# Kernel tuning notes

Measured on AMD Instinct MI355X. Metric: run time of the kernel, lower is better.

Reference implementation:

```python
import jax, jax.numpy as jnp
import numpy as np
import math

B, N, D, H, K, W = 2, 2048, 512, 8, 64, 5
HD = D // H      # head_dim = 64
QC = HD // 4     # per-head quaternion component = 16
QI = D // 4      # full-model quaternion component = 128


def _qlinear(x, r, i, j, k, b):
    # Hamilton-product weight matrix, as built in QLinear.forward
    Wm = jnp.concatenate([
        jnp.concatenate([r, -i, -j, -k], 1),
        jnp.concatenate([i,  r, -k,  j], 1),
        jnp.concatenate([j,  k,  r, -i], 1),
        jnp.concatenate([k, -j,  i,  r], 1)], 0)
    return x @ Wm.T + b


def _layernorm(x, g, b, eps=1e-5):
    m = x.mean(-1, keepdims=True)
    v = ((x - m) ** 2).mean(-1, keepdims=True)
    return (x - m) / jnp.sqrt(v + eps) * g + b


def _forward(query, key, value, cross_context, density_feat, mask, time_idx,
             q_r, q_i, q_j, q_k, q_b, k_r, k_i, k_j, k_k, k_b,
             v_w, v_b, o_w, o_b, thr, dm1_w, dm1_b, dm2_w, dm2_b,
             ef, ec, ev_w, ev_b, ln_g, ln_b):
    spike_slope = 5.0
    # ---- QuaternionSpikeAttention (cross_ctx=True, dropout inactive in eval) ----
    q = _qlinear(query, q_r, q_i, q_j, q_k, q_b)
    k = _qlinear(key, k_r, k_i, k_j, k_k, k_b) + _qlinear(cross_context, k_r, k_i, k_j, k_k, k_b)
    v = jnp.concatenate([value, cross_context], -1) @ v_w.T + v_b
    qh = q.reshape(B, N, H, HD)
    kh = k.reshape(B, N, H, HD)
    vh = v.reshape(B, N, H, HD)
    # sum of the 4 quaternion-component dot products == full dot over head_dim
    scores = jnp.einsum('bmhd,bnhd->bhmn', qh, kh) / math.sqrt(QC)
    scores = jnp.clip(scores, -6.0, 6.0)
    base_thr = jax.nn.softplus(thr)
    hdm = jax.nn.gelu(density_feat @ dm1_w.T + dm1_b, approximate=False)
    d_shift = (hdm @ dm2_w.T + dm2_b)[..., 0]                # [B, N]
    threshold = base_thr + d_shift[:, None, None, :] * 0.1   # varies over key index
    gate = jax.nn.sigmoid(spike_slope * (scores - threshold))
    mod = scores * (1.0 + 2.0 * gate)
    m2 = mask[:, None, :, None] * mask[:, None, None, :]     # [B,1,M,N] outer mask
    mod = jnp.where(m2 == 0, -10000.0, mod)
    wts = jax.nn.softmax(jnp.clip(mod, -30.0, 30.0), axis=-1)
    attn = jnp.einsum('bhmn,bnhd->bmhd', wts, vh).reshape(B, N, D)
    attn = attn @ o_w.T + o_b
    # ---- TemporalEventConvolution ----
    order = jnp.argsort(time_idx, axis=1)
    qs = jnp.take_along_axis(query, order[..., None], axis=1)
    ms = jnp.take_along_axis(mask, order, axis=1)
    half = W // 2
    qp = jnp.pad(qs, ((0, 0), (half, half), (0, 0)))
    qwin = jnp.stack([qp[:, w:w + N] for w in range(W)], axis=2)  # [B,N,W,D]
    # quaternion-split filter matching collapses to a full dot over D
    act = jnp.einsum('bnwd,kwd->bnk', qwin, ef) / math.sqrt(QI)
    act = jnp.where(ms[..., None] == 0, -10000.0, act)
    act = jax.nn.softmax(act, axis=-1)
    ctx = act @ ec                                            # [B,N,D]
    ctx = _layernorm(ctx @ ev_w.T + ev_b, ln_g, ln_b) * ms[..., None]
    inv = jnp.argsort(order, axis=1)
    ctx = jnp.take_along_axis(ctx, inv[..., None], axis=1) * mask[..., None]
    return attn + ctx


def setup_inputs() -> dict:
    key0 = jax.random.key(0)
    ks = jax.random.split(key0, 24)
    lim = math.sqrt(6.0 / (QI + QI))
    def xav(k):
        return jax.random.uniform(k, (QI, QI), jnp.float32, -lim, lim)
    def lin(k, o, i):
        l = math.sqrt(1.0 / i)
        return jax.random.uniform(k, (o, i), jnp.float32, -l, l)
    return {
        'query': jax.random.normal(ks[0], (B, N, D), jnp.float32),
        'key': jax.random.normal(ks[1], (B, N, D), jnp.float32),
        'value': jax.random.normal(ks[2], (B, N, D), jnp.float32),
        'cross_context': jax.random.normal(ks[3], (B, N, D), jnp.float32),
        'density_feat': jax.random.normal(ks[4], (B, N, 3), jnp.float32),
        'mask': jnp.ones((B, N), jnp.float32),
        'time_idx': jax.random.randint(ks[5], (B, N), 0, 1000000),
        'q_r': xav(ks[6]), 'q_i': xav(ks[7]), 'q_j': xav(ks[8]), 'q_k': xav(ks[9]),
        'q_b': jnp.zeros((D,), jnp.float32),
        'k_r': xav(ks[10]), 'k_i': xav(ks[11]), 'k_j': xav(ks[12]), 'k_k': xav(ks[13]),
        'k_b': jnp.zeros((D,), jnp.float32),
        'v_w': lin(ks[14], D, 2 * D), 'v_b': jnp.zeros((D,), jnp.float32),
        'o_w': lin(ks[15], D, D), 'o_b': jnp.zeros((D,), jnp.float32),
        'thr': jnp.float32(-1.0),
        'dm1_w': lin(ks[16], 16, 3), 'dm1_b': jnp.zeros((16,), jnp.float32),
        'dm2_w': jnp.zeros((1, 16), jnp.float32), 'dm2_b': jnp.zeros((1,), jnp.float32),
        'ef': jax.random.normal(ks[17], (K, W, D), jnp.float32) * 0.02,
        'ec': jax.random.normal(ks[18], (K, D), jnp.float32) * 0.02,
        'ev_w': lin(ks[19], D, D), 'ev_b': jnp.zeros((D,), jnp.float32),
        'ln_g': jnp.ones((D,), jnp.float32), 'ln_b': jnp.zeros((D,), jnp.float32),
    }


def reference(query, key, value, cross_context, density_feat, mask, time_idx,
              q_r, q_i, q_j, q_k, q_b, k_r, k_i, k_j, k_k, k_b,
              v_w, v_b, o_w, o_b, thr, dm1_w, dm1_b, dm2_w, dm2_b,
              ef, ec, ev_w, ev_b, ln_g, ln_b):
    return _forward(query, key, value, cross_context, density_feat, mask, time_idx,
                    q_r, q_i, q_j, q_k, q_b, k_r, k_i, k_j, k_k, k_b,
                    v_w, v_b, o_w, o_b, thr, dm1_w, dm1_b, dm2_w, dm2_b,
                    ef, ec, ev_w, ev_b, ln_g, ln_b)
```

## Files before the change

kernel.cpp:

```cpp
#include <hip/hip_runtime.h>
#include <math.h>

#define BB 2
#define NN 2048
#define DDIM 512
#define HH 8
#define HDIM 64
#define BN 4096

#define WS_WMQ   0
#define WS_WMK   262144
#define WS_THRK  524288
#define WS_ORDER 528384
#define WS_DKW   532480
#define WS_W5    1843200
#define WS_Q     2105344
#define WS_K     4202496
#define WS_V     6299648
#define PLANE_US 2097152

typedef short bf16x8 __attribute__((ext_vector_type(8)));
typedef float f32x4  __attribute__((ext_vector_type(4)));

__device__ __forceinline__ float4 ld4(const float* p) { return *(const float4*)p; }

__device__ __forceinline__ float red16_sum(float v) {
  v += __shfl_xor(v, 1, 64);
  v += __shfl_xor(v, 2, 64);
  v += __shfl_xor(v, 4, 64);
  v += __shfl_xor(v, 8, 64);
  return v;
}

__device__ __forceinline__ unsigned short f2bu(float f) {
  unsigned u = __float_as_uint(f);
  unsigned r = 0x7FFFu + ((u >> 16) & 1u);
  return (unsigned short)((u + r) >> 16);
}
__device__ __forceinline__ float bu2f(unsigned short u) {
  return __uint_as_float(((unsigned)u) << 16);
}
__device__ __forceinline__ void split2(float x, unsigned short& hi, unsigned short& lo) {
  hi = f2bu(x);
  lo = f2bu(x - bu2f(hi));
}

__global__ __launch_bounds__(256) void build_wm_kernel(
    const float* __restrict__ qr, const float* __restrict__ qi,
    const float* __restrict__ qj, const float* __restrict__ qk,
    const float* __restrict__ kr, const float* __restrict__ ki,
    const float* __restrict__ kj, const float* __restrict__ kk,
    unsigned short* __restrict__ wmqH, unsigned short* __restrict__ wmqL,
    unsigned short* __restrict__ wmkH, unsigned short* __restrict__ wmkL)
{
  int idx = blockIdx.x * 256 + threadIdx.x;
  int sel = idx >> 18;
  int r   = idx & 262143;
  int p = r >> 9, q = r & 511;
  int pb = p >> 7, qb = q >> 7, pr = p & 127, qc = q & 127;
  const int   comp_t[4][4] = {{0,1,2,3},{1,0,3,2},{2,3,0,1},{3,2,1,0}};
  const float sign_t[4][4] = {{1.f,-1.f,-1.f,-1.f},{1.f,1.f,-1.f,1.f},
                              {1.f,1.f,1.f,-1.f},{1.f,-1.f,1.f,1.f}};
  const float* cq[4] = {qr,qi,qj,qk};
  const float* ck[4] = {kr,ki,kj,kk};
  int c = comp_t[pb][qb];
  float s = sign_t[pb][qb];
  const float* src = sel ? ck[c] : cq[c];
  float v = s * src[pr*128 + qc];
  unsigned short hi, lo;
  split2(v, hi, lo);
  if (sel) { wmkH[r] = hi; wmkL[r] = lo; }
  else     { wmqH[r] = hi; wmqL[r] = lo; }
}

__global__ __launch_bounds__(256) void presplit_kernel(
    const float* __restrict__ src, int n4,
    unsigned short* __restrict__ hp, unsigned short* __restrict__ lp)
{
  int i = blockIdx.x * 256 + threadIdx.x;
  if (i >= n4) return;
  float4 v = ((const float4*)src)[i];
  ushort4 h, l;
  split2(v.x, h.x, l.x);  split2(v.y, h.y, l.y);
  split2(v.z, h.z, l.z);  split2(v.w, h.w, l.w);
  ((ushort4*)hp)[i] = h;
  ((ushort4*)lp)[i] = l;
}

__global__ __launch_bounds__(256) void rank_kernel(const int* __restrict__ tidx,
                                                   int* __restrict__ order)
{
  __shared__ int ts[NN];
  int b = blockIdx.y;
  for (int i = threadIdx.x; i < NN; i += 256) ts[i] = tidx[b*NN + i];
  __syncthreads();
  int i = blockIdx.x * 256 + threadIdx.x;
  int ti = ts[i];
  int rank = 0;
  #pragma unroll 4
  for (int j = 0; j < NN; j++) {
    int tj = ts[j];
    rank += (tj < ti || (tj == ti && j < i)) ? 1 : 0;
  }
  order[b*NN + rank] = i;
}

__global__ __launch_bounds__(256) void thr_kernel(
    const float* __restrict__ df, const float* __restrict__ dm1w,
    const float* __restrict__ dm1b, const float* __restrict__ dm2w,
    const float* __restrict__ dm2b, const float* __restrict__ thrp,
    int dm1b_bstride, float* __restrict__ thrK)
{
  int i = blockIdx.x * 256 + threadIdx.x;
  if (i >= BN) return;
  int b = i >> 11;
  const float* bb = dm1b + b*dm1b_bstride;
  float x0 = df[i*3+0], x1 = df[i*3+1], x2 = df[i*3+2];
  float acc = dm2b[0];
  #pragma unroll
  for (int j = 0; j < 16; j++) {
    float h = dm1w[j*3+0]*x0 + dm1w[j*3+1]*x1 + dm1w[j*3+2]*x2 + bb[j];
    h = 0.5f * h * (1.f + erff(h * 0.70710678118654752f));
    acc += h * dm2w[j];
  }
  float tv = thrp[0];
  float base = fmaxf(tv, 0.f) + log1pf(expf(-fabsf(tv)));
  thrK[i] = base + 0.1f * acc;
}

#define GSTR 72
template<int MODE, int OUT, int AP, int BP>
__global__ __launch_bounds__(256) void mgemm_kernel(
    const float* __restrict__ A0, const float* __restrict__ A1,
    const unsigned short* __restrict__ APh, const unsigned short* __restrict__ APl,
    const float* __restrict__ W,
    const unsigned short* __restrict__ BPh, const unsigned short* __restrict__ BPl,
    const float* __restrict__ bias,
    float bias_scale, float scale, float* __restrict__ out,
    int Ka, int N, int ldout)
{
  __shared__ __align__(16) unsigned short AHi[64*GSTR], ALo[64*GSTR];
  __shared__ __align__(16) unsigned short BHi[64*GSTR], BLo[64*GSTR];
  const int t = threadIdx.x;
  const int w = t >> 6, lane = t & 63;
  const int quad = lane >> 4, lm = lane & 15;
  const int m0 = blockIdx.x * 64, n0 = blockIdx.y * 64;
  const int lrr = t >> 4, ld = (t & 15) * 4;

  f32x4 acc[4];
  #pragma unroll
  for (int s = 0; s < 4; s++) acc[s] = (f32x4){0.f,0.f,0.f,0.f};

  for (int k0 = 0; k0 < Ka; k0 += 64) {
    __syncthreads();
    if (AP) {
      #pragma unroll
      for (int i = 0; i < 2; i++) {
        int c = t*2 + i;
        int row = c >> 3, c8 = (c & 7) * 8;
        int off = (m0 + row)*Ka + k0 + c8;
        *(uint4*)&AHi[row*GSTR + c8] = *(const uint4*)&APh[off];
        *(uint4*)&ALo[row*GSTR + c8] = *(const uint4*)&APl[off];
      }
    } else {
      #pragma unroll
      for (int p = 0; p < 4; p++) {
        int row = lrr + p*16;
        float4 av;
        if (MODE == 0) {
          av = ld4(&A0[(size_t)(m0+row)*Ka + k0 + ld]);
        } else if (MODE == 1) {
          float4 x = ld4(&A0[(m0+row)*512 + k0 + ld]);
          float4 y = ld4(&A1[(m0+row)*512 + k0 + ld]);
          av = make_float4(x.x+y.x, x.y+y.y, x.z+y.z, x.w+y.w);
        } else {
          int kg = k0 + ld;
          av = (kg < 512) ? ld4(&A0[(m0+row)*512 + kg])
                          : ld4(&A1[(m0+row)*512 + kg - 512]);
        }
        ushort4 hi, lo;
        split2(av.x, hi.x, lo.x);  split2(av.y, hi.y, lo.y);
        split2(av.z, hi.z, lo.z);  split2(av.w, hi.w, lo.w);
        *(ushort4*)&AHi[row*GSTR + ld] = hi;
        *(ushort4*)&ALo[row*GSTR + ld] = lo;
      }
    }
    if (BP) {
      #pragma unroll
      for (int i = 0; i < 2; i++) {
        int c = t*2 + i;
        int row = c >> 3, c8 = (c & 7) * 8;
        int brow = n0 + row;  if (brow > N-1) brow = N-1;
        int off = brow*Ka + k0 + c8;
        *(uint4*)&BHi[row*GSTR + c8] = *(const uint4*)&BPh[off];
        *(uint4*)&BLo[row*GSTR + c8] = *(const uint4*)&BPl[off];
      }
    } else {
      #pragma unroll
      for (int p = 0; p < 4; p++) {
        int row = lrr + p*16;
        int brow = n0 + row;  if (brow > N-1) brow = N-1;
        float4 wv = ld4(&W[(size_t)brow*Ka + k0 + ld]);
        ushort4 hi, lo;
        split2(wv.x, hi.x, lo.x);  split2(wv.y, hi.y, lo.y);
        split2(wv.z, hi.z, lo.z);  split2(wv.w, hi.w, lo.w);
        *(ushort4*)&BHi[row*GSTR + ld] = hi;
        *(ushort4*)&BLo[row*GSTR + ld] = lo;
      }
    }
    __syncthreads();
    #pragma unroll
    for (int ks = 0; ks < 2; ks++) {
      int arow = (w*16 + lm)*GSTR + ks*32 + quad*8;
      bf16x8 ah = *(const bf16x8*)&AHi[arow];
      bf16x8 al = *(const bf16x8*)&ALo[arow];
      #pragma unroll
      for (int sub = 0; sub < 4; sub++) {
        int baddr = (sub*16 + lm)*GSTR + ks*32 + quad*8;
        bf16x8 bh = *(const bf16x8*)&BHi[baddr];
        bf16x8 bl = *(const bf16x8*)&BLo[baddr];
        acc[sub] = __builtin_amdgcn_mfma_f32_16x16x32_bf16(ah, bh, acc[sub], 0, 0, 0);
        acc[sub] = __builtin_amdgcn_mfma_f32_16x16x32_bf16(ah, bl, acc[sub], 0, 0, 0);
        acc[sub] = __builtin_amdgcn_mfma_f32_16x16x32_bf16(al, bh, acc[sub], 0, 0, 0);
      }
    }
  }
  #pragma unroll
  for (int sub = 0; sub < 4; sub++) {
    int col = n0 + sub*16 + lm;
    if (col >= N) continue;
    float bv = bias ? bias[col] * bias_scale : 0.f;
    if (OUT == 0) {
      #pragma unroll
      for (int r = 0; r < 4; r++) {
        int row = m0 + w*16 + quad*4 + r;
        out[(size_t)row*ldout + col] = acc[sub][r]*scale + bv;
      }
    } else if (OUT == 1) {
      unsigned short* hp = (unsigned short*)out;
      unsigned short* lp = hp + (size_t)4096*ldout;
      #pragma unroll
      for (int r = 0; r < 4; r++) {
        int row = m0 + w*16 + quad*4 + r;
        unsigned short hv, lv;
        split2(acc[sub][r]*scale + bv, hv, lv);
        hp[(size_t)row*ldout + col] = hv;
        lp[(size_t)row*ldout + col] = lv;
      }
    } else {
      unsigned short* hp = (unsigned short*)out;
      unsigned short* lp = hp + (size_t)PLANE_US;
      int hcol = col >> 6, d = col & 63;
      int row0 = m0 + w*16 + quad*4;
      int bb2 = row0 >> 11, n = row0 & 2047;
      unsigned short h0,h1,h2,h3,l0,l1,l2,l3;
      split2(acc[sub][0]*scale + bv, h0, l0);
      split2(acc[sub][1]*scale + bv, h1, l1);
      split2(acc[sub][2]*scale + bv, h2, l2);
      split2(acc[sub][3]*scale + bv, h3, l3);
      size_t vidx = (((size_t)bb2*8 + hcol)*64 + d)*2048 + n;
      *(ushort4*)&hp[vidx] = make_ushort4(h0,h1,h2,h3);
      *(ushort4*)&lp[vidx] = make_ushort4(l0,l1,l2,l3);
    }
  }
}

__global__ __launch_bounds__(256) void t1a_kernel(const float* __restrict__ dkw,
    const int* __restrict__ order, int K, int W, float* __restrict__ w5raw)
{
  int idx = blockIdx.x * 256 + threadIdx.x;
  if (idx >= BN*K) return;
  int k  = idx % K;
  int bn = idx / K;
  int b = bn >> 11, r = bn & 2047;
  const int* ob = order + b*NN;
  int KW = K*W, half = W >> 1;
  float acc = 0.f;
  for (int w = 0; w < W; w++) {
    int rr = r + w - half;
    if (rr < 0 || rr >= NN) continue;
    acc += dkw[(size_t)(b*NN + ob[rr])*KW + k*W + w];
  }
  w5raw[(size_t)(b*NN + ob[r])*K + k] = acc;
}

__global__ __launch_bounds__(256) void t1b_kernel(const float* __restrict__ mask,
    int K, float* __restrict__ w5)
{
  int i = blockIdx.x * 256 + threadIdx.x;
  if (i >= BN) return;
  float* row = w5 + (size_t)i*K;
  if (mask[i] == 0.f) {
    float u = 1.f / (float)K;
    for (int k = 0; k < K; k++) row[k] = u;
    return;
  }
  float mx = -1e30f;
  for (int k = 0; k < K; k++) mx = fmaxf(mx, row[k]);
  float ss = 0.f;
  for (int k = 0; k < K; k++) { float e = __expf(row[k]-mx); row[k] = e; ss += e; }
  float inv = 1.f/ss;
  for (int k = 0; k < K; k++) row[k] *= inv;
}

__global__ __launch_bounds__(256) void ecv_kernel(const float* __restrict__ ec,
    const float* __restrict__ evw, int K, float* __restrict__ ecv)
{
  int idx = blockIdx.x * 256 + threadIdx.x;
  if (idx >= K*512) return;
  int k = idx >> 9, j = idx & 511;
  const float4* e4 = (const float4*)(ec + k*512);
  const float4* w4 = (const float4*)(evw + j*512);
  float acc = 0.f;
  for (int d = 0; d < 128; d++) {
    float4 a = e4[d], b = w4[d];
    acc += a.x*b.x + a.y*b.y + a.z*b.z + a.w*b.w;
  }
  ecv[k*512 + j] = acc;
}

__global__ __launch_bounds__(256) void t2p_kernel(const float* __restrict__ w5,
    const float* __restrict__ ecv, const float* __restrict__ evb,
    int K, float* __restrict__ ctx2)
{
  int idx = blockIdx.x * 256 + threadIdx.x;
  int bn = idx >> 7;
  int q4 = idx & 127;
  const float* wp = w5 + (size_t)bn*K;
  const float4* e4 = (const float4*)ecv;
  float4 bv = ((const float4*)evb)[q4];
  float4 acc = bv;
  for (int k = 0; k < K; k++) {
    float w = wp[k];
    float4 e = e4[k*128 + q4];
    acc.x += w*e.x; acc.y += w*e.y; acc.z += w*e.z; acc.w += w*e.w;
  }
  ((float4*)ctx2)[idx] = acc;
}

#define QSTR 72
__global__ __launch_bounds__(256) void attn_kernel(
    const unsigned short* __restrict__ QHi, const unsigned short* __restrict__ QLo,
    const unsigned short* __restrict__ KHp, const unsigned short* __restrict__ KLp,
    const unsigned short* __restrict__ VtHi, const unsigned short* __restrict__ VtLo,
    const float* __restrict__ thrK, const float* __restrict__ mask,
    unsigned short* __restrict__ AoutH, unsigned short* __restrict__ AoutL)
{
  __shared__ __align__(16) unsigned short KHs[64*QSTR];
  __shared__ __align__(16) unsigned short KLs[64*QSTR];
  __shared__ __align__(16) unsigned short VHs[64*QSTR];
  __shared__ __align__(16) unsigned short VLs[64*QSTR];
  __shared__ float thr_s[64], mk_s[64], mm_s[32];
  __shared__ float ls[2][32];

  const int t = threadIdx.x;
  const int wv = t >> 6, lane = t & 63;
  const int g = wv & 1, sh = wv >> 1;
  const int quad = lane >> 4, lm = lane & 15;
  const int m0 = blockIdx.x * 32;
  const int bh = blockIdx.y;
  const int b = bh >> 3, h = bh & 7;
  const int base = b*NN*DDIM + h*HDIM;
  const int sr = t >> 3;
  const int sc = (t & 7) * 8;

  bf16x8 qh[2], ql[2];
  {
    size_t qoff = (size_t)(b*NN + m0 + g*16 + lm)*DDIM + h*HDIM + quad*8;
    qh[0] = *(const bf16x8*)&QHi[qoff];
    qh[1] = *(const bf16x8*)&QHi[qoff + 32];
    ql[0] = *(const bf16x8*)&QLo[qoff];
    ql[1] = *(const bf16x8*)&QLo[qoff + 32];
  }
  if (t < 32) mm_s[t] = mask[b*NN + m0 + t];

  f32x4 o_acc[2];
  o_acc[0] = (f32x4){0.f,0.f,0.f,0.f};
  o_acc[1] = (f32x4){0.f,0.f,0.f,0.f};
  float lsum[4] = {0.f,0.f,0.f,0.f};

  for (int n0 = 0; n0 < NN; n0 += 64) {
    __syncthreads();
    #pragma unroll
    for (int p = 0; p < 2; p++) {
      int row = sr + p*32;
      size_t gg = (size_t)(b*NN + n0 + row)*DDIM + h*HDIM + sc;
      *(uint4*)&KHs[row*QSTR + sc] = *(const uint4*)&KHp[gg];
      *(uint4*)&KLs[row*QSTR + sc] = *(const uint4*)&KLp[gg];
      size_t gv = ((size_t)bh*HDIM + row)*NN + n0 + sc;
      *(uint4*)&VHs[row*QSTR + sc] = *(const uint4*)&VtHi[gv];
      *(uint4*)&VLs[row*QSTR + sc] = *(const uint4*)&VtLo[gv];
    }
    if (t < 64) { thr_s[t] = thrK[b*NN + n0 + t]; mk_s[t] = mask[b*NN + n0 + t]; }
    __syncthreads();

    f32x4 s_acc[2];
    s_acc[0] = (f32x4){0.f,0.f,0.f,0.f};
    s_acc[1] = (f32x4){0.f,0.f,0.f,0.f};
    #pragma unroll
    for (int ks = 0; ks < 2; ks++) {
      #pragma unroll
      for (int sl = 0; sl < 2; sl++) {
        int sub = sh*2 + sl;
        int baddr = (sub*16 + lm)*QSTR + ks*32 + quad*8;
        bf16x8 bh8 = *(const bf16x8*)&KHs[baddr];
        bf16x8 bl8 = *(const bf16x8*)&KLs[baddr];
        s_acc[sl] = __builtin_amdgcn_mfma_f32_16x16x32_bf16(qh[ks], bh8, s_acc[sl], 0, 0, 0);
        s_acc[sl] = __builtin_amdgcn_mfma_f32_16x16x32_bf16(qh[ks], bl8, s_acc[sl], 0, 0, 0);
        s_acc[sl] = __builtin_amdgcn_mfma_f32_16x16x32_bf16(ql[ks], bh8, s_acc[sl], 0, 0, 0);
      }
    }
    __syncthreads();

    float thc5[2], mkc[2];
    #pragma unroll
    for (int sl = 0; sl < 2; sl++) {
      int key = (sh*2 + sl)*16 + lm;
      thc5[sl] = 5.f * thr_s[key];
      mkc[sl] = mk_s[key];
    }
    float p_[4][2];
    #pragma unroll
    for (int r = 0; r < 4; r++) {
      float mm = mm_s[g*16 + quad*4 + r];
      #pragma unroll
      for (int sl = 0; sl < 2; sl++) {
        float sc2 = s_acc[sl][r]*0.25f;
        sc2 = fminf(fmaxf(sc2,-6.f),6.f);
        float e = __expf(__builtin_fmaf(-5.f, sc2, thc5[sl]));
        float gte = __builtin_amdgcn_rcpf(1.f + e);
        float mv = sc2*(1.f + 2.f*gte);
        if (mm*mkc[sl] == 0.f) mv = -1e4f;
        mv = fminf(fmaxf(mv,-30.f),30.f);
        float p = __expf(mv - 30.f);
        p_[r][sl] = p;
        lsum[r] += p;
      }
    }
    #pragma unroll
    for (int r = 0; r < 4; r++) {
      int prow = (g*16 + quad*4 + r)*QSTR;
      int xk = quad << 3;
      #pragma unroll
      for (int sl = 0; sl < 2; sl++) {
        int cx = (lm + (sh*2+sl)*16) ^ xk;
        unsigned short hi, lo;
        split2(p_[r][sl], hi, lo);
        KHs[prow + cx] = hi;
        KLs[prow + cx] = lo;
      }
    }
    __syncthreads();

    bf16x8 ph[2], pl[2];
    {
      int arow = (g*16 + lm)*QSTR;
      int rk = ((lm >> 2) & 3) << 3;
      int c0 = (quad*8) ^ rk;
      int c1 = (quad*8 + 32) ^ rk;
      ph[0] = *(const bf16x8*)&KHs[arow + c0];
      ph[1] = *(const bf16x8*)&KHs[arow + c1];
      pl[0] = *(const bf16x8*)&KLs[arow + c0];
      pl[1] = *(const bf16x8*)&KLs[arow + c1];
    }
    #pragma unroll
    for (int ks = 0; ks < 2; ks++) {
      #pragma unroll
      for (int sl = 0; sl < 2; sl++) {
        int sub = sh*2 + sl;
        int baddr = (sub*16 + lm)*QSTR + ks*32 + quad*8;
        bf16x8 vh8 = *(const bf16x8*)&VHs[baddr];
        bf16x8 vl8 = *(const bf16x8*)&VLs[baddr];
        o_acc[sl] = __builtin_amdgcn_mfma_f32_16x16x32_bf16(ph[ks], vh8, o_acc[sl], 0, 0, 0);
        o_acc[sl] = __builtin_amdgcn_mfma_f32_16x16x32_bf16(ph[ks], vl8, o_acc[sl], 0, 0, 0);
        o_acc[sl] = __builtin_amdgcn_mfma_f32_16x16x32_bf16(pl[ks], vh8, o_acc[sl], 0, 0, 0);
      }
    }
  }

  __syncthreads();
  #pragma unroll
  for (int r = 0; r < 4; r++) {
    float s = red16_sum(lsum[r]);
    if (lm == 0) ls[sh][g*16 + quad*4 + r] = s;
  }
  __syncthreads();
  float inv[4];
  #pragma unroll
  for (int r = 0; r < 4; r++) {
    int rl = g*16 + quad*4 + r;
    inv[r] = 1.f / (ls[0][rl] + ls[1][rl]);
  }
  #pragma unroll
  for (int sl = 0; sl < 2; sl++) {
    #pragma unroll
    for (int r = 0; r < 4; r++) {
      int row = m0 + g*16 + quad*4 + r;
      float val = o_acc[sl][r] * inv[r];
      unsigned short hv, lv;
      split2(val, hv, lv);
      size_t o = (size_t)base + (size_t)row*DDIM + (sh*2+sl)*16 + lm;
      AoutH[o] = hv;
      AoutL[o] = lv;
    }
  }
}

__global__ __launch_bounds__(256) void t3_kernel(const float* __restrict__ ctx2,
    const float* __restrict__ lng, const float* __restrict__ lnb,
    const float* __restrict__ mask, const float* __restrict__ outf,
    float* __restrict__ out)
{
  int wid = threadIdx.x >> 6, lane = threadIdx.x & 63;
  int row = blockIdx.x * 4 + wid;
  const float4* x4 = (const float4*)(ctx2 + row*DDIM);
  float4 v0 = x4[lane], v1 = x4[lane+64];
  float s = v0.x+v0.y+v0.z+v0.w + v1.x+v1.y+v1.z+v1.w;
  #pragma unroll
  for (int m = 1; m < 64; m <<= 1) s += __shfl_xor(s, m, 64);
  float mean = s * (1.f/512.f);
  float d0 = v0.x-mean, d1 = v0.y-mean, d2 = v0.z-mean, d3 = v0.w-mean;
  float d4 = v1.x-mean, d5 = v1.y-mean, d6 = v1.z-mean, d7 = v1.w-mean;
  float sq = d0*d0+d1*d1+d2*d2+d3*d3+d4*d4+d5*d5+d6*d6+d7*d7;
  #pragma unroll
  for (int m = 1; m < 64; m <<= 1) sq += __shfl_xor(sq, m, 64);
  float rstd = rsqrtf(sq * (1.f/512.f) + 1e-5f);
  float mk = mask[row];
  float f = mk*mk;
  const float4* g4 = (const float4*)lng;
  const float4* b4 = (const float4*)lnb;
  float4 G0 = g4[lane], G1 = g4[lane+64], B0 = b4[lane], B1 = b4[lane+64];
  float4 O0 = *(const float4*)&outf[row*DDIM + lane*4];
  float4 O1 = *(const float4*)&outf[row*DDIM + (lane+64)*4];
  float4 R0, R1;
  R0.x = O0.x + (d0*rstd*G0.x + B0.x)*f;
  R0.y = O0.y + (d1*rstd*G0.y + B0.y)*f;
  R0.z = O0.z + (d2*rstd*G0.z + B0.z)*f;
  R0.w = O0.w + (d3*rstd*G0.w + B0.w)*f;
  R1.x = O1.x + (d4*rstd*G1.x + B1.x)*f;
  R1.y = O1.y + (d5*rstd*G1.y + B1.y)*f;
  R1.z = O1.z + (d6*rstd*G1.z + B1.z)*f;
  R1.w = O1.w + (d7*rstd*G1.w + B1.w)*f;
  *(float4*)&out[row*DDIM + lane*4] = R0;
  *(float4*)&out[row*DDIM + (lane+64)*4] = R1;
}

__global__ void telem_write_kernel(float val, float* __restrict__ out)
{
  if (threadIdx.x == 0 && blockIdx.x == 0) out[0] = val;
}

extern "C" void kernel_launch(void* const* d_in, const int* in_sizes, int n_in,
                              void* d_out, int out_size, void* d_ws, size_t ws_size,
                              hipStream_t stream)
{
  (void)n_in; (void)out_size; (void)ws_size;
  const float* query = (const float*)d_in[0];
  const float* key_  = (const float*)d_in[1];
  const float* value = (const float*)d_in[2];
  const float* cross = (const float*)d_in[3];
  const float* df    = (const float*)d_in[4];
  const float* mask  = (const float*)d_in[5];
  const int*   tidx  = (const int*)  d_in[6];
  const float* q_r = (const float*)d_in[7],  *q_i = (const float*)d_in[8];
  const float* q_j = (const float*)d_in[9],  *q_k = (const float*)d_in[10];
  const float* q_b = (const float*)d_in[11];
  const float* k_r = (const float*)d_in[12], *k_i = (const float*)d_in[13];
  const float* k_j = (const float*)d_in[14], *k_k = (const float*)d_in[15];
  const float* k_b = (const float*)d_in[16];
  const float* v_w = (const float*)d_in[17], *v_b = (const float*)d_in[18];
  const float* o_w = (const float*)d_in[19], *o_b = (const float*)d_in[20];
  const float* thrp = (const float*)d_in[21];
  const float* dm1w = (const float*)d_in[22], *dm1b = (const float*)d_in[23];
  const float* dm2w = (const float*)d_in[24], *dm2b = (const float*)d_in[25];
  const float* ef   = (const float*)d_in[26], *ec   = (const float*)d_in[27];
  const float* ev_w = (const float*)d_in[28], *ev_b = (const float*)d_in[29];
  const float* lng  = (const float*)d_in[30], *lnb  = (const float*)d_in[31];

  const int s23 = in_sizes[23];
  const int s26 = in_sizes[26];
  const int s27 = in_sizes[27];
  int Kf = (s27 > 0 && s27 % 512 == 0) ? s27 / 512 : 0;
  int Wf = (Kf > 0 && s26 % (Kf*512) == 0) ? s26 / (Kf*512) : 0;
  bool cfg_ok = (Kf >= 1 && Kf <= 64) && (Wf == 1 || Wf == 3 || Wf == 5)
                && (Kf*Wf <= 320);
  if (!cfg_ok) { Kf = 5; Wf = 5; }
  const int KW = Kf * Wf;
  const int dm1b_bstride = (s23 == 32) ? 16 : 0;

  float* ws   = (float*)d_ws;
  float* thrK = ws + WS_THRK;
  int*   order = (int*)(ws + WS_ORDER);
  float* dkw  = ws + WS_DKW;
  float* w5   = ws + WS_W5;
  float* Qb   = ws + WS_Q;
  float* Kb   = ws + WS_K;
  float* Vb   = ws + WS_V;
  float* out  = (float*)d_out;
  float* OutF = Kb;
  float* ctx2 = Qb;

  unsigned short* wmqH = (unsigned short*)(ws + WS_WMQ);
  unsigned short* wmqL = wmqH + 262144;
  unsigned short* wmkH = (unsigned short*)(ws + WS_WMK);
  unsigned short* wmkL = wmkH + 262144;
  unsigned short* qryH = (unsigned short*)d_out;
  unsigned short* qryL = qryH + PLANE_US;
  unsigned short* vwH  = (unsigned short*)(ws + WS_DKW);
  unsigned short* vwL  = vwH + 524288;
  unsigned short* owH  = (unsigned short*)(ws + WS_W5);
  unsigned short* owL  = owH + 262144;
  unsigned short* efH  = (unsigned short*)(ws + WS_WMQ);
  unsigned short* efL  = efH + KW*512;
  float* ecv = ws + WS_WMQ;

  const unsigned short* QHi = (const unsigned short*)Qb;
  const unsigned short* QLo = QHi + PLANE_US;
  const unsigned short* KHp = (const unsigned short*)Kb;
  const unsigned short* KLp = KHp + PLANE_US;
  const unsigned short* VtH = (const unsigned short*)Vb;
  const unsigned short* VtL = VtH + PLANE_US;

  build_wm_kernel<<<2048, 256, 0, stream>>>(q_r,q_i,q_j,q_k, k_r,k_i,k_j,k_k,
                                            wmqH, wmqL, wmkH, wmkL);
  rank_kernel<<<dim3(8,2), 256, 0, stream>>>(tidx, order);
  thr_kernel<<<16, 256, 0, stream>>>(df, dm1w, dm1b, dm2w, dm2b, thrp,
                                     dm1b_bstride, thrK);
  presplit_kernel<<<2048, 256, 0, stream>>>(query, 524288, qryH, qryL);
  presplit_kernel<<<512, 256, 0, stream>>>(v_w, 131072, vwH, vwL);
  presplit_kernel<<<256, 256, 0, stream>>>(o_w, 65536, owH, owL);

  const float rs128 = 0.08838834764831845f;
  mgemm_kernel<0,1,1,1><<<dim3(64,8), 256, 0, stream>>>(
      nullptr, nullptr, qryH, qryL, nullptr, wmqH, wmqL, q_b, 1.f, 1.f, Qb, 512, 512, 512);
  mgemm_kernel<1,1,0,1><<<dim3(64,8), 256, 0, stream>>>(
      key_, cross, nullptr, nullptr, nullptr, wmkH, wmkL, k_b, 2.f, 1.f, Kb, 512, 512, 512);
  presplit_kernel<<<(KW*128 + 255)/256, 256, 0, stream>>>(ef, KW*128, efH, efL);
  mgemm_kernel<2,2,0,1><<<dim3(64,8), 256, 0, stream>>>(
      value, cross, nullptr, nullptr, nullptr, vwH, vwL, v_b, 1.f, 1.f, Vb, 1024, 512, 512);
  mgemm_kernel<0,0,1,1><<<dim3(64,(KW+63)/64), 256, 0, stream>>>(
      nullptr, nullptr, qryH, qryL, nullptr, efH, efL, nullptr, 0.f, rs128, dkw, 512, KW, KW);

  attn_kernel<<<dim3(64,16), 256, 0, stream>>>(QHi, QLo, KHp, KLp, VtH, VtL,
                                               thrK, mask, qryH, qryL);
  mgemm_kernel<0,0,1,1><<<dim3(64,8), 256, 0, stream>>>(
      nullptr, nullptr, qryH, qryL, nullptr, owH, owL, o_b, 1.f, 1.f, OutF, 512, 512, 512);

  t1a_kernel<<<(BN*Kf + 255)/256, 256, 0, stream>>>(dkw, order, Kf, Wf, w5);
  t1b_kernel<<<16, 256, 0, stream>>>(mask, Kf, w5);
  ecv_kernel<<<(Kf*512 + 255)/256, 256, 0, stream>>>(ec, ev_w, Kf, ecv);
  t2p_kernel<<<2048, 256, 0, stream>>>(w5, ecv, ev_b, Kf, ctx2);
  t3_kernel<<<1024, 256, 0, stream>>>(ctx2, lng, lnb, mask, OutF, out);

  if (!cfg_ok) {
    int K2 = (s27 / 512 < 127) ? s27 / 512 : 127;
    telem_write_kernel<<<1, 64, 0, stream>>>(-65536.f * (float)(K2+1), out);
  }
}
```

Before: 546.1 us.

## Register-prefetch next tiles in GEMM and attention loops

Both the split-bf16 GEMM kernel and the attention kernel now load the next K-tile (and V/threshold/mask tiles) from global memory into registers while the current tile is being computed from LDS. The stores to shared memory happen at the top of each iteration from the prefetched registers. This hides global-load latency behind MFMA work, at the cost of more registers per thread and a possible drop in occupancy.

```diff
diff --git a/kernel.cpp b/kernel.cpp
--- a/kernel.cpp
+++ b/kernel.cpp
@@ -147,36 +147,75 @@
   const int m0 = blockIdx.x * 64, n0 = blockIdx.y * 64;
   const int lrr = t >> 4, ld = (t & 15) * 4;
 
-  f32x4 acc[4];
-  #pragma unroll
-  for (int s = 0; s < 4; s++) acc[s] = (f32x4){0.f,0.f,0.f,0.f};
-
-  for (int k0 = 0; k0 < Ka; k0 += 64) {
-    __syncthreads();
+  uint4  raH[2], raL[2];
+  float4 rfA[4], rfA2[4];
+  uint4  rbH[2], rbL[2];
+  float4 rfB[4];
+
+  auto loadA = [&](int kk) {
     if (AP) {
       #pragma unroll
       for (int i = 0; i < 2; i++) {
         int c = t*2 + i;
         int row = c >> 3, c8 = (c & 7) * 8;
-        int off = (m0 + row)*Ka + k0 + c8;
-        *(uint4*)&AHi[row*GSTR + c8] = *(const uint4*)&APh[off];
-        *(uint4*)&ALo[row*GSTR + c8] = *(const uint4*)&APl[off];
+        int off = (m0 + row)*Ka + kk + c8;
+        raH[i] = *(const uint4*)&APh[off];
+        raL[i] = *(const uint4*)&APl[off];
       }
     } else {
       #pragma unroll
       for (int p = 0; p < 4; p++) {
         int row = lrr + p*16;
-        float4 av;
         if (MODE == 0) {
-          av = ld4(&A0[(size_t)(m0+row)*Ka + k0 + ld]);
+          rfA[p] = ld4(&A0[(size_t)(m0+row)*Ka + kk + ld]);
         } else if (MODE == 1) {
-          float4 x = ld4(&A0[(m0+row)*512 + k0 + ld]);
-          float4 y = ld4(&A1[(m0+row)*512 + k0 + ld]);
-          av = make_float4(x.x+y.x, x.y+y.y, x.z+y.z, x.w+y.w);
+          rfA[p]  = ld4(&A0[(m0+row)*512 + kk + ld]);
+          rfA2[p] = ld4(&A1[(m0+row)*512 + kk + ld]);
         } else {
-          int kg = k0 + ld;
-          av = (kg < 512) ? ld4(&A0[(m0+row)*512 + kg])
-                          : ld4(&A1[(m0+row)*512 + kg - 512]);
+          int kg = kk + ld;
+          rfA[p] = (kg < 512) ? ld4(&A0[(m0+row)*512 + kg])
+                              : ld4(&A1[(m0+row)*512 + kg - 512]);
+        }
+      }
+    }
+  };
+  auto loadB = [&](int kk) {
+    if (BP) {
+      #pragma unroll
+      for (int i = 0; i < 2; i++) {
+        int c = t*2 + i;
+        int row = c >> 3, c8 = (c & 7) * 8;
+        int brow = n0 + row;  if (brow > N-1) brow = N-1;
+        int off = brow*Ka + kk + c8;
+        rbH[i] = *(const uint4*)&BPh[off];
+        rbL[i] = *(const uint4*)&BPl[off];
+      }
+    } else {
+      #pragma unroll
+      for (int p = 0; p < 4; p++) {
+        int row = lrr + p*16;
+        int brow = n0 + row;  if (brow > N-1) brow = N-1;
+        rfB[p] = ld4(&W[(size_t)brow*Ka + kk + ld]);
+      }
+    }
+  };
+  auto storeA = [&]() {
+    if (AP) {
+      #pragma unroll
+      for (int i = 0; i < 2; i++) {
+        int c = t*2 + i;
+        int row = c >> 3, c8 = (c & 7) * 8;
+        *(uint4*)&AHi[row*GSTR + c8] = raH[i];
+        *(uint4*)&ALo[row*GSTR + c8] = raL[i];
+      }
+    } else {
+      #pragma unroll
+      for (int p = 0; p < 4; p++) {
+        int row = lrr + p*16;
+        float4 av = rfA[p];
+        if (MODE == 1) {
+          float4 y = rfA2[p];
+          av = make_float4(av.x+y.x, av.y+y.y, av.z+y.z, av.w+y.w);
         }
         ushort4 hi, lo;
         split2(av.x, hi.x, lo.x);  split2(av.y, hi.y, lo.y);
@@ -185,29 +224,39 @@
         *(ushort4*)&ALo[row*GSTR + ld] = lo;
       }
     }
+  };
+  auto storeB = [&]() {
     if (BP) {
       #pragma unroll
       for (int i = 0; i < 2; i++) {
         int c = t*2 + i;
         int row = c >> 3, c8 = (c & 7) * 8;
-        int brow = n0 + row;  if (brow > N-1) brow = N-1;
-        int off = brow*Ka + k0 + c8;
-        *(uint4*)&BHi[row*GSTR + c8] = *(const uint4*)&BPh[off];
-        *(uint4*)&BLo[row*GSTR + c8] = *(const uint4*)&BPl[off];
+        *(uint4*)&BHi[row*GSTR + c8] = rbH[i];
+        *(uint4*)&BLo[row*GSTR + c8] = rbL[i];
       }
     } else {
       #pragma unroll
       for (int p = 0; p < 4; p++) {
         int row = lrr + p*16;
-        int brow = n0 + row;  if (brow > N-1) brow = N-1;
-        float4 wv = ld4(&W[(size_t)brow*Ka + k0 + ld]);
         ushort4 hi, lo;
-        split2(wv.x, hi.x, lo.x);  split2(wv.y, hi.y, lo.y);
-        split2(wv.z, hi.z, lo.z);  split2(wv.w, hi.w, lo.w);
+        split2(rfB[p].x, hi.x, lo.x);  split2(rfB[p].y, hi.y, lo.y);
+        split2(rfB[p].z, hi.z, lo.z);  split2(rfB[p].w, hi.w, lo.w);
         *(ushort4*)&BHi[row*GSTR + ld] = hi;
         *(ushort4*)&BLo[row*GSTR + ld] = lo;
       }
     }
+  };
+
+  f32x4 acc[4];
+  #pragma unroll
+  for (int s = 0; s < 4; s++) acc[s] = (f32x4){0.f,0.f,0.f,0.f};
+
+  loadA(0); loadB(0);
+  for (int k0 = 0; k0 < Ka; k0 += 64) {
+    __syncthreads();
+    storeA(); storeB();
+    int kn = (k0 + 64 < Ka) ? k0 + 64 : k0;
+    loadA(kn); loadB(kn);
     __syncthreads();
     #pragma unroll
     for (int ks = 0; ks < 2; ks++) {
@@ -379,19 +428,45 @@
   o_acc[1] = (f32x4){0.f,0.f,0.f,0.f};
   float lsum[4] = {0.f,0.f,0.f,0.f};
 
-  for (int n0 = 0; n0 < NN; n0 += 64) {
+  uint4 rKH[2], rKL[2], rVH[2], rVL[2];
+  float rthr = 0.f, rmk = 0.f;
+  #pragma unroll
+  for (int p = 0; p < 2; p++) {
+    int row = sr + p*32;
+    size_t gg = (size_t)(b*NN + row)*DDIM + h*HDIM + sc;
+    rKH[p] = *(const uint4*)&KHp[gg];
+    rKL[p] = *(const uint4*)&KLp[gg];
+    size_t gv = ((size_t)bh*HDIM + row)*NN + sc;
+    rVH[p] = *(const uint4*)&VtHi[gv];
+    rVL[p] = *(const uint4*)&VtLo[gv];
+  }
+  if (t < 64) { rthr = thrK[b*NN + t]; rmk = mask[b*NN + t]; }
+
+  for (int it = 0; it < 32; it++) {
     __syncthreads();
     #pragma unroll
     for (int p = 0; p < 2; p++) {
       int row = sr + p*32;
-      size_t gg = (size_t)(b*NN + n0 + row)*DDIM + h*HDIM + sc;
-      *(uint4*)&KHs[row*QSTR + sc] = *(const uint4*)&KHp[gg];
-      *(uint4*)&KLs[row*QSTR + sc] = *(const uint4*)&KLp[gg];
-      size_t gv = ((size_t)bh*HDIM + row)*NN + n0 + sc;
-      *(uint4*)&VHs[row*QSTR + sc] = *(const uint4*)&VtHi[gv];
-      *(uint4*)&VLs[row*QSTR + sc] = *(const uint4*)&VtLo[gv];
-    }
-    if (t < 64) { thr_s[t] = thrK[b*NN + n0 + t]; mk_s[t] = mask[b*NN + n0 + t]; }
+      *(uint4*)&KHs[row*QSTR + sc] = rKH[p];
+      *(uint4*)&KLs[row*QSTR + sc] = rKL[p];
+      *(uint4*)&VHs[row*QSTR + sc] = rVH[p];
+      *(uint4*)&VLs[row*QSTR + sc] = rVL[p];
+    }
+    if (t < 64) { thr_s[t] = rthr; mk_s[t] = rmk; }
+    {
+      int n1 = (it < 31) ? (it+1)*64 : 0;
+      #pragma unroll
+      for (int p = 0; p < 2; p++) {
+        int row = sr + p*32;
+        size_t gg = (size_t)(b*NN + n1 + row)*DDIM + h*HDIM + sc;
+        rKH[p] = *(const uint4*)&KHp[gg];
+        rKL[p] = *(const uint4*)&KLp[gg];
+        size_t gv = ((size_t)bh*HDIM + row)*NN + n1 + sc;
+        rVH[p] = *(const uint4*)&VtHi[gv];
+        rVL[p] = *(const uint4*)&VtLo[gv];
+      }
+      if (t < 64) { rthr = thrK[b*NN + n1 + t]; rmk = mask[b*NN + n1 + t]; }
+    }
     __syncthreads();
 
     f32x4 s_acc[2];
```

Measured after the change: 890.0 us. +63.0%, slower.
